# Optimization experiments

Measured on AMD Instinct MI355X. Metric: run time of the kernel, lower is better.

Reference implementation:

```python
import jax, jax.numpy as jnp
import numpy as np

S, B, E, H, DFF = 1024, 8, 1024, 16, 4096
D = E // H
EPS = 1e-5


def _layernorm(x, g, b):
    m = jnp.mean(x, axis=-1, keepdims=True)
    v = jnp.mean(jnp.square(x - m), axis=-1, keepdims=True)
    return (x - m) * jax.lax.rsqrt(v + EPS) * g + b


def setup_inputs() -> dict:
    key = jax.random.key(0)
    ks = jax.random.split(key, 6)
    return {
        "src": jax.random.normal(ks[0], (S, B, E), jnp.float32),
        "in_proj_w": jax.random.normal(ks[1], (3 * E, E), jnp.float32) * (E ** -0.5),
        "in_proj_b": jnp.zeros((3 * E,), jnp.float32),
        "out_w": jax.random.normal(ks[2], (E, E), jnp.float32) * (E ** -0.5),
        "out_b": jnp.zeros((E,), jnp.float32),
        "ln1_g": jnp.ones((E,), jnp.float32),
        "ln1_b": jnp.zeros((E,), jnp.float32),
        "ln2_g": jnp.ones((E,), jnp.float32),
        "ln2_b": jnp.zeros((E,), jnp.float32),
        "w1": jax.random.normal(ks[3], (DFF, E), jnp.float32) * (E ** -0.5),
        "b1": jnp.zeros((DFF,), jnp.float32),
        "w2": jax.random.normal(ks[4], (E, DFF), jnp.float32) * (DFF ** -0.5),
        "b2": jnp.zeros((E,), jnp.float32),
    }


def reference(src, in_proj_w, in_proj_b, out_w, out_b, ln1_g, ln1_b, ln2_g, ln2_b, w1, b1, w2, b2):
    # src: (S, B, E). Packed in-projection: qkv = src @ W^T + b, split into q,k,v.
    qkv = src @ in_proj_w.T + in_proj_b          # (S, B, 3E)
    q, k, v = jnp.split(qkv, 3, axis=-1)
    q = q.reshape(S, B, H, D)
    k = k.reshape(S, B, H, D)
    v = v.reshape(S, B, H, D)
    # Torch scales q by 1/sqrt(head_dim) before the bmm.
    scores = jnp.einsum("sbhd,tbhd->bhst", q * (D ** -0.5), k)   # (B, H, S, S)
    attn = jax.nn.softmax(scores, axis=-1)
    ctx = jnp.einsum("bhst,tbhd->sbhd", attn, v).reshape(S, B, E)
    attn_out = ctx @ out_w.T + out_b
    # Post-norm encoder layer (norm_first=False), dropout=0.
    x = _layernorm(src + attn_out, ln1_g, ln1_b)
    ff = jax.nn.relu(x @ w1.T + b1) @ w2.T + b2
    return _layernorm(x + ff, ln2_g, ln2_b)
```

## Files before the change

### kernel.cpp

```cpp
#include <hip/hip_runtime.h>

#define S_LEN 1024
#define BATCH 8
#define EMB   1024
#define NH    16
#define HD    64
#define FFD   4096
#define ROWS  (S_LEN*BATCH)

typedef __attribute__((ext_vector_type(8))) short  short8;
typedef __attribute__((ext_vector_type(4))) float  float4v;
typedef __attribute__((ext_vector_type(4))) unsigned int uint4v;

struct alignas(8) us4 { unsigned short x, y, z, w; };

__device__ __forceinline__ unsigned short f2bf(float f) {
    unsigned int u = __float_as_uint(f);
    u += 0x7fffu + ((u >> 16) & 1u);
    return (unsigned short)(u >> 16);
}
__device__ __forceinline__ float bf2f(unsigned short b) {
    return __uint_as_float((unsigned int)b << 16);
}
__device__ __forceinline__ unsigned int cvtpk_bf16(float lo, float hi) {
    unsigned int r;
    asm("v_cvt_pk_bf16_f32 %0, %1, %2" : "=v"(r) : "v"(lo), "v"(hi));
    return r;
}
__device__ __forceinline__ float exp2v(float x) {
    float r;
    asm("v_exp_f32 %0, %1" : "=v"(r) : "v"(x));
    return r;
}

__device__ __forceinline__ void gload_lds16(const void* g, void* l) {
    __builtin_amdgcn_global_load_lds(
        (const __attribute__((address_space(1))) unsigned int*)g,
        (__attribute__((address_space(3))) unsigned int*)l, 16, 0, 0);
}

__device__ __forceinline__ int swz(int row, int chunk) {
    return (row << 7) + ((chunk ^ (row & 7)) << 4);
}

__device__ __forceinline__ void xcd_decode(int id, int& lx, int& ly) {
    int k = id & 7, j = id >> 3;
    ly = k * 4 + (j & 3);
    lx = j >> 2;
}

__global__ __launch_bounds__(256) void cast_all(const float* __restrict__ s0, unsigned short* __restrict__ d0, int n0,
                                                const float* __restrict__ s1, unsigned short* __restrict__ d1, int n1,
                                                const float* __restrict__ s2, unsigned short* __restrict__ d2, int n2,
                                                const float* __restrict__ s3, unsigned short* __restrict__ d3, int n3,
                                                const float* __restrict__ s4, unsigned short* __restrict__ d4, int n4) {
    int i = blockIdx.x * 256 + threadIdx.x;
    const float* s; unsigned short* d;
    if (i < n0)                { s = s0; d = d0; }
    else if ((i -= n0) < n1)   { s = s1; d = d1; }
    else if ((i -= n1) < n2)   { s = s2; d = d2; }
    else if ((i -= n2) < n3)   { s = s3; d = d3; }
    else if ((i -= n3) < n4)   { s = s4; d = d4; }
    else return;
    float4 v = ((const float4*)s)[i];
    us4 o = { f2bf(v.x), f2bf(v.y), f2bf(v.z), f2bf(v.w) };
    ((us4*)d)[i] = o;
}

#define QSCALE 0.18033688011112042f
template <int MODE>
__global__ __launch_bounds__(512, 2) void gemm256(const unsigned short* __restrict__ A,
                                                  const unsigned short* __restrict__ Bw,
                                                  const float* __restrict__ bias,
                                                  unsigned short* __restrict__ outb,
                                                  int M, int N, int K) {
    __shared__ char lds[131072];
    const int tid = threadIdx.x, lane = tid & 63, w = tid >> 6;
    const int wr = w >> 2, wc = w & 3;
    int lx, ly;
    xcd_decode(blockIdx.x, lx, ly);
    const int m0 = ly * 256, n0 = lx * 256;
    const int nt = K >> 6;

    size_t baseA[2], baseB[2];
    int ldsOff[2];
#pragma unroll
    for (int q = 0; q < 2; ++q) {
        int ci = q * 512 + tid;
        int row = ci >> 3;
        int c = (ci & 7) ^ (row & 7);
        baseA[q] = (size_t)(m0 + row) * K + c * 8;
        baseB[q] = (size_t)(n0 + row) * K + c * 8;
        ldsOff[q] = ci * 16;
    }

    auto stage = [&](int kt, int which) {
        int ktc = kt < nt ? kt : 0;
        int slot = kt & 1;
        if (which < 2) {
#pragma unroll
            for (int q = 0; q < 2; ++q)
                gload_lds16(A + baseA[q] + (size_t)which * 128 * K + (size_t)ktc * 64,
                            lds + slot * 32768 + which * 16384 + ldsOff[q]);
        } else {
            int h = which - 2;
#pragma unroll
            for (int q = 0; q < 2; ++q)
                gload_lds16(Bw + baseB[q] + (size_t)h * 128 * K + (size_t)ktc * 64,
                            lds + 65536 + slot * 32768 + h * 16384 + ldsOff[q]);
        }
    };

    auto rdA = [&](int slot, int mh, int i, int mk) -> short8 {
        int arow = wr * 128 + mh * 64 + i * 16 + (lane & 15);
        return *(const short8*)(lds + slot * 32768 + swz(arow, mk * 4 + (lane >> 4)));
    };
    auto rdB = [&](int slot, int nh, int j, int mk) -> short8 {
        int brow = wc * 64 + nh * 32 + j * 16 + (lane & 15);
        return *(const short8*)(lds + 65536 + slot * 32768 + swz(brow, mk * 4 + (lane >> 4)));
    };

    float4v acc[8][4];
#pragma unroll
    for (int i = 0; i < 8; ++i)
#pragma unroll
        for (int j = 0; j < 4; ++j) acc[i][j] = (float4v){0.f, 0.f, 0.f, 0.f};

    short8 a[4][2], b[2][2][2];

    stage(0, 0); stage(0, 1); stage(0, 2); stage(0, 3);
    stage(1, 0);
    asm volatile("s_waitcnt vmcnt(2)" ::: "memory");
    __builtin_amdgcn_s_barrier();

#define MFMA16(MH, NH)                                                          \
    __builtin_amdgcn_s_setprio(1);                                              \
    _Pragma("unroll")                                                           \
    for (int i = 0; i < 4; ++i)                                                 \
        _Pragma("unroll")                                                       \
        for (int j = 0; j < 2; ++j) {                                           \
            acc[(MH)*4+i][(NH)*2+j] = __builtin_amdgcn_mfma_f32_16x16x32_bf16(  \
                a[i][0], b[NH][j][0], acc[(MH)*4+i][(NH)*2+j], 0, 0, 0);        \
            acc[(MH)*4+i][(NH)*2+j] = __builtin_amdgcn_mfma_f32_16x16x32_bf16(  \
                a[i][1], b[NH][j][1], acc[(MH)*4+i][(NH)*2+j], 0, 0, 0);        \
        }                                                                       \
    __builtin_amdgcn_s_setprio(0);

    for (int t = 0; t < nt; ++t) {
        const int slot = t & 1;
#pragma unroll
        for (int i = 0; i < 4; ++i) {
            a[i][0] = rdA(slot, 0, i, 0);
            a[i][1] = rdA(slot, 0, i, 1);
        }
#pragma unroll
        for (int j = 0; j < 2; ++j) {
            b[0][j][0] = rdB(slot, 0, j, 0);
            b[0][j][1] = rdB(slot, 0, j, 1);
        }
        stage(t + 1, 1);
        __builtin_amdgcn_s_barrier();
        asm volatile("s_waitcnt lgkmcnt(0)" ::: "memory");
        __builtin_amdgcn_sched_barrier(0);
        MFMA16(0, 0)
        __builtin_amdgcn_s_barrier();
#pragma unroll
        for (int j = 0; j < 2; ++j) {
            b[1][j][0] = rdB(slot, 1, j, 0);
            b[1][j][1] = rdB(slot, 1, j, 1);
        }
        stage(t + 1, 2);
        __builtin_amdgcn_s_barrier();
        asm volatile("s_waitcnt lgkmcnt(0)" ::: "memory");
        __builtin_amdgcn_sched_barrier(0);
        MFMA16(0, 1)
        __builtin_amdgcn_s_barrier();
#pragma unroll
        for (int i = 0; i < 4; ++i) {
            a[i][0] = rdA(slot, 1, i, 0);
            a[i][1] = rdA(slot, 1, i, 1);
        }
        stage(t + 1, 3);
        __builtin_amdgcn_s_barrier();
        asm volatile("s_waitcnt lgkmcnt(0)" ::: "memory");
        __builtin_amdgcn_sched_barrier(0);
        MFMA16(1, 1)
        __builtin_amdgcn_s_barrier();
        stage(t + 2, 0);
        MFMA16(1, 0)
        asm volatile("s_waitcnt vmcnt(2)" ::: "memory");
        __builtin_amdgcn_s_barrier();
    }
#undef MFMA16
    asm volatile("s_waitcnt vmcnt(0)" ::: "memory");

#pragma unroll
    for (int mi = 0; mi < 8; ++mi) {
#pragma unroll
        for (int nj = 0; nj < 4; ++nj) {
            int col = n0 + wc * 64 + nj * 16 + (lane & 15);
            float bv = bias[col];
#pragma unroll
            for (int r = 0; r < 4; ++r) {
                int row = m0 + wr * 128 + mi * 16 + (lane >> 4) * 4 + r;
                size_t idx = (size_t)row * N + col;
                float v = acc[mi][nj][r] + bv;
                if (MODE == 0) {
                    if (col < EMB) v *= QSCALE;
                    outb[idx] = f2bf(v);
                } else {
                    outb[idx] = f2bf(fmaxf(v, 0.f));
                }
            }
        }
    }
}

template <int MODE>
__global__ __launch_bounds__(512, 2) void gemm256n(const unsigned short* __restrict__ A,
                                                   const unsigned short* __restrict__ Bw,
                                                   const float* __restrict__ bias,
                                                   const float* __restrict__ res,
                                                   const unsigned short* __restrict__ resb,
                                                   float* __restrict__ outf,
                                                   int M, int N, int K) {
    __shared__ char lds[147456];
    const int tid = threadIdx.x, lane = tid & 63, w = tid >> 6;
    const int wr = w >> 1, wc = w & 1;
    int lx, ly;
    xcd_decode(blockIdx.x, lx, ly);
    const int m0 = ly * 256, n0 = lx * 128;
    const int nt = K >> 6;
    const int g = lane >> 4, qs = lane & 15;

    size_t baseA[4], baseB[2];
    int ldsOffA[4], ldsOffB[2];
#pragma unroll
    for (int q = 0; q < 4; ++q) {
        int ci = q * 512 + tid;
        int row = ci >> 3;
        int c = (ci & 7) ^ (row & 7);
        baseA[q] = (size_t)(m0 + row) * K + c * 8;
        ldsOffA[q] = ci * 16;
    }
#pragma unroll
    for (int q = 0; q < 2; ++q) {
        int ci = q * 512 + tid;
        int row = ci >> 3;
        int c = (ci & 7) ^ (row & 7);
        baseB[q] = (size_t)(n0 + row) * K + c * 8;
        ldsOffB[q] = ci * 16;
    }

    auto stage = [&](int kt) {
        int ktc = kt < nt ? kt : 0;
        int slot = kt % 3;
#pragma unroll
        for (int q = 0; q < 4; ++q)
            gload_lds16(A + baseA[q] + (size_t)ktc * 64,
                        lds + slot * 32768 + ldsOffA[q]);
#pragma unroll
        for (int q = 0; q < 2; ++q)
            gload_lds16(Bw + baseB[q] + (size_t)ktc * 64,
                        lds + 98304 + slot * 16384 + ldsOffB[q]);
    };

    auto rdA = [&](int slot, int i, int mk) -> short8 {
        int arow = wr * 64 + i * 16 + qs;
        return *(const short8*)(lds + slot * 32768 + swz(arow, mk * 4 + g));
    };
    auto rdB = [&](int slot, int j, int mk) -> short8 {
        int brow = wc * 64 + j * 16 + qs;
        return *(const short8*)(lds + 98304 + slot * 16384 + swz(brow, mk * 4 + g));
    };

    float4v acc[4][4];
#pragma unroll
    for (int i = 0; i < 4; ++i)
#pragma unroll
        for (int j = 0; j < 4; ++j) acc[i][j] = (float4v){0.f, 0.f, 0.f, 0.f};

    short8 a[4][2], b[4][2];

    stage(0); stage(1);
    asm volatile("s_waitcnt vmcnt(6)" ::: "memory");
    __builtin_amdgcn_s_barrier();

    for (int t = 0; t < nt; ++t) {
        const int slot = t % 3;
#pragma unroll
        for (int i = 0; i < 4; ++i) {
            a[i][0] = rdA(slot, i, 0);
            a[i][1] = rdA(slot, i, 1);
        }
#pragma unroll
        for (int j = 0; j < 4; ++j) {
            b[j][0] = rdB(slot, j, 0);
            b[j][1] = rdB(slot, j, 1);
        }
        stage(t + 2);
        asm volatile("s_waitcnt lgkmcnt(0)" ::: "memory");
        __builtin_amdgcn_sched_barrier(0);
        __builtin_amdgcn_s_setprio(1);
#pragma unroll
        for (int i = 0; i < 4; ++i)
#pragma unroll
            for (int j = 0; j < 4; ++j) {
                acc[i][j] = __builtin_amdgcn_mfma_f32_16x16x32_bf16(
                    a[i][0], b[j][0], acc[i][j], 0, 0, 0);
                acc[i][j] = __builtin_amdgcn_mfma_f32_16x16x32_bf16(
                    a[i][1], b[j][1], acc[i][j], 0, 0, 0);
            }
        __builtin_amdgcn_s_setprio(0);
        asm volatile("s_waitcnt vmcnt(6)" ::: "memory");
        __builtin_amdgcn_s_barrier();
    }
    asm volatile("s_waitcnt vmcnt(0)" ::: "memory");

#pragma unroll
    for (int mi = 0; mi < 4; ++mi) {
#pragma unroll
        for (int j = 0; j < 4; ++j) {
            int col = n0 + wc * 64 + j * 16 + qs;
            float bv = bias[col];
#pragma unroll
            for (int r = 0; r < 4; ++r) {
                int row = m0 + wr * 64 + mi * 16 + g * 4 + r;
                size_t idx = (size_t)row * N + col;
                float v = acc[mi][j][r] + bv;
                if (MODE == 1) outf[idx] = v + res[idx];
                else           outf[idx] = v + bf2f(resb[idx]);
            }
        }
    }
}

__global__ __launch_bounds__(256) void vtrans(const unsigned short* __restrict__ qkv,
                                              unsigned short* __restrict__ vt) {
    const int bh = blockIdx.y, b = bh >> 4, h = bh & 15;
    const int t0 = blockIdx.x * 64;
    const int tid = threadIdx.x;
    __shared__ unsigned short lds[64][72];
#pragma unroll
    for (int rep = 0; rep < 2; ++rep) {
        int slot = rep * 256 + tid;
        int row = slot >> 3, cc = slot & 7;
        const unsigned short* g =
            qkv + ((size_t)(t0 + row) * BATCH + b) * 3072 + 2 * EMB + h * 64 + cc * 8;
        *(uint4v*)&lds[row][cc * 8] = *(const uint4v*)g;
    }
    __syncthreads();
#pragma unroll
    for (int rep = 0; rep < 2; ++rep) {
        int slot = rep * 256 + tid;
        int d = slot >> 3, tc = slot & 7;
        unsigned short tmp[8] __attribute__((aligned(16)));
#pragma unroll
        for (int j = 0; j < 8; ++j) tmp[j] = lds[tc * 8 + j][d];
        unsigned short* g = vt + ((size_t)bh * 64 + d) * S_LEN + t0 + tc * 8;
        *(uint4v*)g = *(const uint4v*)tmp;
    }
}

__global__ __launch_bounds__(256, 6) void attn(const unsigned short* __restrict__ qkv,
                                               const unsigned short* __restrict__ vt,
                                               unsigned short* __restrict__ ctx) {
    __shared__ char Ks[64 * 128];
    __shared__ char Vs[64 * 128];
    __shared__ char QP[64 * 128];
    const int tid = threadIdx.x, lane = tid & 63, w = tid >> 6;
    const int bh = blockIdx.x & 127, b = bh >> 4, h = bh & 15;
    const int s0 = (blockIdx.x >> 7) * 64;
    const int g = lane >> 4, qs = lane & 15;

#pragma unroll
    for (int p = 0; p < 2; ++p) {
        int ci = p * 256 + tid;
        int row = ci >> 3, c = (ci & 7) ^ (row & 7);
        gload_lds16(qkv + ((size_t)(s0 + row) * BATCH + b) * 3072 + h * 64 + c * 8,
                    QP + (p * 256 + w * 64) * 16);
    }
    __syncthreads();

    short8 qa0 = *(const short8*)(QP + swz(w * 16 + qs, 0 * 4 + g));
    short8 qa1 = *(const short8*)(QP + swz(w * 16 + qs, 1 * 4 + g));
    asm volatile("s_waitcnt lgkmcnt(0)" ::: "memory");
    __builtin_amdgcn_sched_barrier(0);
    char* Ps = QP + w * 2048;

    float4v O[4];
#pragma unroll
    for (int df = 0; df < 4; ++df) O[df] = (float4v){0.f, 0.f, 0.f, 0.f};
    float m_s = -1e30f;
    float l_s = 0.f;

    for (int t0 = 0; t0 < S_LEN; t0 += 64) {
        __syncthreads();
#pragma unroll
        for (int p = 0; p < 2; ++p) {
            int ci = p * 256 + tid;
            int row = ci >> 3, c = (ci & 7) ^ (row & 7);
            gload_lds16(qkv + ((size_t)(t0 + row) * BATCH + b) * 3072 + EMB + h * 64 + c * 8,
                        Ks + (p * 256 + w * 64) * 16);
            gload_lds16(vt + ((size_t)bh * 64 + row) * S_LEN + t0 + c * 8,
                        Vs + (p * 256 + w * 64) * 16);
        }
        __syncthreads();

        float4v Sf[4];
#pragma unroll
        for (int tf = 0; tf < 4; ++tf) Sf[tf] = (float4v){0.f, 0.f, 0.f, 0.f};
#pragma unroll
        for (int tf = 0; tf < 4; ++tf) {
            int kr = tf * 16 + qs;
            short8 kb0 = *(const short8*)(Ks + swz(kr, 0 * 4 + g));
            short8 kb1 = *(const short8*)(Ks + swz(kr, 1 * 4 + g));
            Sf[tf] = __builtin_amdgcn_mfma_f32_16x16x32_bf16(kb0, qa0, Sf[tf], 0, 0, 0);
            Sf[tf] = __builtin_amdgcn_mfma_f32_16x16x32_bf16(kb1, qa1, Sf[tf], 0, 0, 0);
        }

        float mx = fmaxf(fmaxf(Sf[0][0], Sf[0][1]), fmaxf(Sf[0][2], Sf[0][3]));
#pragma unroll
        for (int tf = 1; tf < 4; ++tf)
            mx = fmaxf(mx, fmaxf(fmaxf(Sf[tf][0], Sf[tf][1]),
                                 fmaxf(Sf[tf][2], Sf[tf][3])));
        mx = fmaxf(mx, __shfl_xor(mx, 16));
        mx = fmaxf(mx, __shfl_xor(mx, 32));

        if (!__all(mx - m_s <= 8.0f)) {
            float mnew = fmaxf(m_s, mx);
            float alpha = exp2v(m_s - mnew);
            m_s = mnew;
            l_s *= alpha;
#pragma unroll
            for (int r = 0; r < 4; ++r) {
                float ar = __shfl(alpha, 4 * g + r);
#pragma unroll
                for (int df = 0; df < 4; ++df) O[df][r] *= ar;
            }
        }

        float rs = 0.f;
#pragma unroll
        for (int tf = 0; tf < 4; ++tf) {
            float p0 = exp2v(Sf[tf][0] - m_s);
            float p1 = exp2v(Sf[tf][1] - m_s);
            float p2 = exp2v(Sf[tf][2] - m_s);
            float p3 = exp2v(Sf[tf][3] - m_s);
            rs += (p0 + p1) + (p2 + p3);
            uint2 pk = make_uint2(cvtpk_bf16(p0, p1), cvtpk_bf16(p2, p3));
            *(uint2*)(Ps + (qs << 7) +
                      (((2 * tf + (g >> 1)) ^ (qs & 7)) << 4) + ((g & 1) << 3)) = pk;
        }
        rs += __shfl_xor(rs, 16);
        rs += __shfl_xor(rs, 32);
        l_s += rs;

        asm volatile("s_waitcnt lgkmcnt(0)" ::: "memory");
        __builtin_amdgcn_sched_barrier(0);

#pragma unroll
        for (int mk = 0; mk < 2; ++mk) {
            short8 pa = *(const short8*)(Ps + swz(qs, mk * 4 + g));
#pragma unroll
            for (int df = 0; df < 4; ++df) {
                int vr = df * 16 + qs;
                short8 vb = *(const short8*)(Vs + swz(vr, mk * 4 + g));
                O[df] = __builtin_amdgcn_mfma_f32_16x16x32_bf16(pa, vb, O[df], 0, 0, 0);
            }
        }
    }

    float inv = __builtin_amdgcn_rcpf(l_s);
#pragma unroll
    for (int r = 0; r < 4; ++r) {
        float ir = __shfl(inv, 4 * g + r);
#pragma unroll
        for (int df = 0; df < 4; ++df) {
            int srow = s0 + w * 16 + g * 4 + r;
            int d    = df * 16 + qs;
            ctx[((size_t)srow * BATCH + b) * EMB + h * 64 + d] = f2bf(O[df][r] * ir);
        }
    }
}

__global__ __launch_bounds__(256) void ln_ker(const float* __restrict__ y,
                                              const float* __restrict__ g,
                                              const float* __restrict__ bta,
                                              float* __restrict__ xo,
                                              unsigned short* __restrict__ xb) {
    const int row = blockIdx.x, tid = threadIdx.x, lane = tid & 63, w = tid >> 6;
    float4 v = ((const float4*)(y + (size_t)row * EMB))[tid];
    float s = v.x + v.y + v.z + v.w;
    float q = v.x * v.x + v.y * v.y + v.z * v.z + v.w * v.w;
#pragma unroll
    for (int m = 1; m < 64; m <<= 1) {
        s += __shfl_xor(s, m);
        q += __shfl_xor(q, m);
    }
    __shared__ float ps[4], pq[4];
    if (lane == 0) { ps[w] = s; pq[w] = q; }
    __syncthreads();
    s = ps[0] + ps[1] + ps[2] + ps[3];
    q = pq[0] + pq[1] + pq[2] + pq[3];
    float mean = s * (1.f / EMB);
    float var  = q * (1.f / EMB) - mean * mean;
    float rstd = rsqrtf(var + 1e-5f);
    float4 gv = ((const float4*)g)[tid];
    float4 bv = ((const float4*)bta)[tid];
    float4 o;
    o.x = (v.x - mean) * rstd * gv.x + bv.x;
    o.y = (v.y - mean) * rstd * gv.y + bv.y;
    o.z = (v.z - mean) * rstd * gv.z + bv.z;
    o.w = (v.w - mean) * rstd * gv.w + bv.w;
    if (xo) ((float4*)(xo + (size_t)row * EMB))[tid] = o;
    if (xb) {
        us4 ob = { f2bf(o.x), f2bf(o.y), f2bf(o.z), f2bf(o.w) };
        ((us4*)(xb + (size_t)row * EMB))[tid] = ob;
    }
}

extern "C" void kernel_launch(void* const* d_in, const int* in_sizes, int n_in,
                              void* d_out, int out_size, void* d_ws, size_t ws_size,
                              hipStream_t stream) {
    (void)in_sizes; (void)n_in; (void)out_size;
    const float* src       = (const float*)d_in[0];
    const float* in_proj_w = (const float*)d_in[1];
    const float* in_proj_b = (const float*)d_in[2];
    const float* out_w     = (const float*)d_in[3];
    const float* out_b     = (const float*)d_in[4];
    const float* ln1_g     = (const float*)d_in[5];
    const float* ln1_b     = (const float*)d_in[6];
    const float* ln2_g     = (const float*)d_in[7];
    const float* ln2_b     = (const float*)d_in[8];
    const float* w1        = (const float*)d_in[9];
    const float* b1        = (const float*)d_in[10];
    const float* w2        = (const float*)d_in[11];
    const float* b2        = (const float*)d_in[12];

    const size_t MB = 1u << 20;
    if (ws_size < 104 * MB) return;

    char* ws = (char*)d_ws;
    unsigned short* wqkvb = (unsigned short*)(ws);
    unsigned short* wob   = (unsigned short*)(ws + 6 * MB);
    unsigned short* w1b   = (unsigned short*)(ws + 8 * MB);
    unsigned short* w2b   = (unsigned short*)(ws + 16 * MB);
    unsigned short* qkvb  = (unsigned short*)(ws + 24 * MB);
    unsigned short* srcbf = (unsigned short*)(ws + 72 * MB);
    unsigned short* vtb   = (unsigned short*)(ws + 88 * MB);
    unsigned short* ctxb  = (unsigned short*)(ws + 72 * MB);
    unsigned short* xbf   = (unsigned short*)(ws + 24 * MB);
    unsigned short* hb    = (unsigned short*)(ws + 40 * MB);
    float*          yout  = (float*)d_out;

    const int c0 = ROWS * EMB / 4;
    const int c1 = 3 * EMB * EMB / 4;
    const int c2 = EMB * EMB / 4;
    const int c3 = FFD * EMB / 4;
    const int c4 = EMB * FFD / 4;
    const int ctot = c0 + c1 + c2 + c3 + c4;
    cast_all<<<ctot / 256, 256, 0, stream>>>(
        src, srcbf, c0, in_proj_w, wqkvb, c1, out_w, wob, c2,
        w1, w1b, c3, w2, w2b, c4);

    gemm256<0><<<(3 * EMB / 256) * 32, 512, 0, stream>>>(
        srcbf, wqkvb, in_proj_b, qkvb, ROWS, 3 * EMB, EMB);

    vtrans<<<dim3(S_LEN / 64, BATCH * NH), 256, 0, stream>>>(qkvb, vtb);

    attn<<<(S_LEN / 64) * BATCH * NH, 256, 0, stream>>>(qkvb, vtb, ctxb);

    gemm256n<1><<<(EMB / 128) * 32, 512, 0, stream>>>(
        ctxb, wob, out_b, src, nullptr, yout, ROWS, EMB, EMB);

    ln_ker<<<ROWS, 256, 0, stream>>>(yout, ln1_g, ln1_b, nullptr, xbf);

    gemm256<2><<<(FFD / 256) * 32, 512, 0, stream>>>(
        xbf, w1b, b1, hb, ROWS, FFD, EMB);

    gemm256n<3><<<(EMB / 128) * 32, 512, 0, stream>>>(
        hb, w2b, b2, nullptr, xbf, yout, ROWS, EMB, FFD);

    ln_ker<<<ROWS, 256, 0, stream>>>(yout, ln2_g, ln2_b, (float*)d_out, nullptr);
}
```

Measured before the change: 325.7 us.

## Triple-buffer A tile and cut barriers in 256x256 GEMM main loop

Replaces the 256x256 bf16 GEMM's four-phase loop, which had several barriers per k-step, with a loop that has one barrier per k-step. The A tile is triple-buffered and B double-buffered, using 160 KB of LDS, so loads run two steps ahead for A. Each wave now loads all four B fragments at once and runs two 32-MFMA bursts, reloading only the A fragments between them. This trades more LDS (160 KB) and more live registers for fewer synchronisations and deeper prefetch, and assumes the LDS allocation still fits on the device.

```diff
diff --git a/kernel.cpp b/kernel.cpp
--- a/kernel.cpp
+++ b/kernel.cpp
@@ -69,23 +69,24 @@
 
 #define QSCALE 0.18033688011112042f
 template <int MODE>
-__global__ __launch_bounds__(512, 2) void gemm256(const unsigned short* __restrict__ A,
-                                                  const unsigned short* __restrict__ Bw,
-                                                  const float* __restrict__ bias,
-                                                  unsigned short* __restrict__ outb,
-                                                  int M, int N, int K) {
-    __shared__ char lds[131072];
+__global__ __launch_bounds__(512, 2) void gemm256d(const unsigned short* __restrict__ A,
+                                                   const unsigned short* __restrict__ Bw,
+                                                   const float* __restrict__ bias,
+                                                   unsigned short* __restrict__ outb,
+                                                   int M, int N, int K) {
+    __shared__ char lds[163840];
     const int tid = threadIdx.x, lane = tid & 63, w = tid >> 6;
     const int wr = w >> 2, wc = w & 3;
+    const int g = lane >> 4, qs = lane & 15;
     int lx, ly;
     xcd_decode(blockIdx.x, lx, ly);
     const int m0 = ly * 256, n0 = lx * 256;
     const int nt = K >> 6;
 
-    size_t baseA[2], baseB[2];
-    int ldsOff[2];
-#pragma unroll
-    for (int q = 0; q < 2; ++q) {
+    size_t baseA[4], baseB[4];
+    int ldsOff[4];
+#pragma unroll
+    for (int q = 0; q < 4; ++q) {
         int ci = q * 512 + tid;
         int row = ci >> 3;
         int c = (ci & 7) ^ (row & 7);
@@ -94,30 +95,30 @@
         ldsOff[q] = ci * 16;
     }
 
-    auto stage = [&](int kt, int which) {
+    auto stageA = [&](int kt) {
+        int ktc = kt < nt ? kt : 0;
+        int slot = kt % 3;
+#pragma unroll
+        for (int q = 0; q < 4; ++q)
+            gload_lds16(A + baseA[q] + (size_t)ktc * 64,
+                        lds + slot * 32768 + ldsOff[q]);
+    };
+    auto stageB = [&](int kt) {
         int ktc = kt < nt ? kt : 0;
         int slot = kt & 1;
-        if (which < 2) {
-#pragma unroll
-            for (int q = 0; q < 2; ++q)
-                gload_lds16(A + baseA[q] + (size_t)which * 128 * K + (size_t)ktc * 64,
-                            lds + slot * 32768 + which * 16384 + ldsOff[q]);
-        } else {
-            int h = which - 2;
-#pragma unroll
-            for (int q = 0; q < 2; ++q)
-                gload_lds16(Bw + baseB[q] + (size_t)h * 128 * K + (size_t)ktc * 64,
-                            lds + 65536 + slot * 32768 + h * 16384 + ldsOff[q]);
-        }
-    };
-
-    auto rdA = [&](int slot, int mh, int i, int mk) -> short8 {
-        int arow = wr * 128 + mh * 64 + i * 16 + (lane & 15);
-        return *(const short8*)(lds + slot * 32768 + swz(arow, mk * 4 + (lane >> 4)));
-    };
-    auto rdB = [&](int slot, int nh, int j, int mk) -> short8 {
-        int brow = wc * 64 + nh * 32 + j * 16 + (lane & 15);
-        return *(const short8*)(lds + 65536 + slot * 32768 + swz(brow, mk * 4 + (lane >> 4)));
+#pragma unroll
+        for (int q = 0; q < 4; ++q)
+            gload_lds16(Bw + baseB[q] + (size_t)ktc * 64,
+                        lds + 98304 + slot * 32768 + ldsOff[q]);
+    };
+
+    auto rdA = [&](int slot, int ig, int mk) -> short8 {
+        int arow = wr * 128 + ig * 16 + qs;
+        return *(const short8*)(lds + slot * 32768 + swz(arow, mk * 4 + g));
+    };
+    auto rdB = [&](int slot, int j, int mk) -> short8 {
+        int brow = wc * 64 + j * 16 + qs;
+        return *(const short8*)(lds + 98304 + slot * 32768 + swz(brow, mk * 4 + g));
     };
 
     float4v acc[8][4];
@@ -126,83 +127,71 @@
 #pragma unroll
         for (int j = 0; j < 4; ++j) acc[i][j] = (float4v){0.f, 0.f, 0.f, 0.f};
 
-    short8 a[4][2], b[2][2][2];
-
-    stage(0, 0); stage(0, 1); stage(0, 2); stage(0, 3);
-    stage(1, 0);
-    asm volatile("s_waitcnt vmcnt(2)" ::: "memory");
+    short8 a[4][2], b[4][2];
+
+    stageA(0); stageB(0); stageA(1);
+    asm volatile("s_waitcnt vmcnt(4)" ::: "memory");
     __builtin_amdgcn_s_barrier();
 
-#define MFMA16(MH, NH)                                                          \
-    __builtin_amdgcn_s_setprio(1);                                              \
-    _Pragma("unroll")                                                           \
-    for (int i = 0; i < 4; ++i)                                                 \
-        _Pragma("unroll")                                                       \
-        for (int j = 0; j < 2; ++j) {                                           \
-            acc[(MH)*4+i][(NH)*2+j] = __builtin_amdgcn_mfma_f32_16x16x32_bf16(  \
-                a[i][0], b[NH][j][0], acc[(MH)*4+i][(NH)*2+j], 0, 0, 0);        \
-            acc[(MH)*4+i][(NH)*2+j] = __builtin_amdgcn_mfma_f32_16x16x32_bf16(  \
-                a[i][1], b[NH][j][1], acc[(MH)*4+i][(NH)*2+j], 0, 0, 0);        \
-        }                                                                       \
-    __builtin_amdgcn_s_setprio(0);
-
     for (int t = 0; t < nt; ++t) {
-        const int slot = t & 1;
+        const int sa = t % 3, sb = t & 1;
 #pragma unroll
         for (int i = 0; i < 4; ++i) {
-            a[i][0] = rdA(slot, 0, i, 0);
-            a[i][1] = rdA(slot, 0, i, 1);
-        }
-#pragma unroll
-        for (int j = 0; j < 2; ++j) {
-            b[0][j][0] = rdB(slot, 0, j, 0);
-            b[0][j][1] = rdB(slot, 0, j, 1);
-        }
-        stage(t + 1, 1);
-        __builtin_amdgcn_s_barrier();
+            a[i][0] = rdA(sa, i, 0);
+            a[i][1] = rdA(sa, i, 1);
+        }
+#pragma unroll
+        for (int j = 0; j < 4; ++j) {
+            b[j][0] = rdB(sb, j, 0);
+            b[j][1] = rdB(sb, j, 1);
+        }
+        stageB(t + 1);
+        stageA(t + 2);
         asm volatile("s_waitcnt lgkmcnt(0)" ::: "memory");
         __builtin_amdgcn_sched_barrier(0);
-        MFMA16(0, 0)
-        __builtin_amdgcn_s_barrier();
-#pragma unroll
-        for (int j = 0; j < 2; ++j) {
-            b[1][j][0] = rdB(slot, 1, j, 0);
-            b[1][j][1] = rdB(slot, 1, j, 1);
-        }
-        stage(t + 1, 2);
-        __builtin_amdgcn_s_barrier();
+        __builtin_amdgcn_s_setprio(1);
+#pragma unroll
+        for (int i = 0; i < 4; ++i)
+#pragma unroll
+            for (int j = 0; j < 4; ++j) {
+                acc[i][j] = __builtin_amdgcn_mfma_f32_16x16x32_bf16(
+                    a[i][0], b[j][0], acc[i][j], 0, 0, 0);
+                acc[i][j] = __builtin_amdgcn_mfma_f32_16x16x32_bf16(
+                    a[i][1], b[j][1], acc[i][j], 0, 0, 0);
+            }
+        __builtin_amdgcn_s_setprio(0);
+#pragma unroll
+        for (int i = 0; i < 4; ++i) {
+            a[i][0] = rdA(sa, 4 + i, 0);
+            a[i][1] = rdA(sa, 4 + i, 1);
+        }
         asm volatile("s_waitcnt lgkmcnt(0)" ::: "memory");
         __builtin_amdgcn_sched_barrier(0);
-        MFMA16(0, 1)
+        __builtin_amdgcn_s_setprio(1);
+#pragma unroll
+        for (int i = 0; i < 4; ++i)
+#pragma unroll
+            for (int j = 0; j < 4; ++j) {
+                acc[4 + i][j] = __builtin_amdgcn_mfma_f32_16x16x32_bf16(
+                    a[i][0], b[j][0], acc[4 + i][j], 0, 0, 0);
+                acc[4 + i][j] = __builtin_amdgcn_mfma_f32_16x16x32_bf16(
+                    a[i][1], b[j][1], acc[4 + i][j], 0, 0, 0);
+            }
+        __builtin_amdgcn_s_setprio(0);
+        asm volatile("s_waitcnt vmcnt(4)" ::: "memory");
         __builtin_amdgcn_s_barrier();
-#pragma unroll
-        for (int i = 0; i < 4; ++i) {
-            a[i][0] = rdA(slot, 1, i, 0);
-            a[i][1] = rdA(slot, 1, i, 1);
-        }
-        stage(t + 1, 3);
-        __builtin_amdgcn_s_barrier();
-        asm volatile("s_waitcnt lgkmcnt(0)" ::: "memory");
-        __builtin_amdgcn_sched_barrier(0);
-        MFMA16(1, 1)
-        __builtin_amdgcn_s_barrier();
-        stage(t + 2, 0);
-        MFMA16(1, 0)
-        asm volatile("s_waitcnt vmcnt(2)" ::: "memory");
-        __builtin_amdgcn_s_barrier();
-    }
-#undef MFMA16
+    }
     asm volatile("s_waitcnt vmcnt(0)" ::: "memory");
 
 #pragma unroll
     for (int mi = 0; mi < 8; ++mi) {
 #pragma unroll
         for (int nj = 0; nj < 4; ++nj) {
-            int col = n0 + wc * 64 + nj * 16 + (lane & 15);
+            int col = n0 + wc * 64 + nj * 16 + qs;
             float bv = bias[col];
 #pragma unroll
             for (int r = 0; r < 4; ++r) {
-                int row = m0 + wr * 128 + mi * 16 + (lane >> 4) * 4 + r;
+                int row = m0 + wr * 128 + mi * 16 + g * 4 + r;
                 size_t idx = (size_t)row * N + col;
                 float v = acc[mi][nj][r] + bv;
                 if (MODE == 0) {
@@ -564,7 +553,7 @@
         src, srcbf, c0, in_proj_w, wqkvb, c1, out_w, wob, c2,
         w1, w1b, c3, w2, w2b, c4);
 
-    gemm256<0><<<(3 * EMB / 256) * 32, 512, 0, stream>>>(
+    gemm256d<0><<<(3 * EMB / 256) * 32, 512, 0, stream>>>(
         srcbf, wqkvb, in_proj_b, qkvb, ROWS, 3 * EMB, EMB);
 
     vtrans<<<dim3(S_LEN / 64, BATCH * NH), 256, 0, stream>>>(qkvb, vtb);
@@ -576,7 +565,7 @@
 
     ln_ker<<<ROWS, 256, 0, stream>>>(yout, ln1_g, ln1_b, nullptr, xbf);
 
-    gemm256<2><<<(FFD / 256) * 32, 512, 0, stream>>>(
+    gemm256d<2><<<(FFD / 256) * 32, 512, 0, stream>>>(
         xbf, w1b, b1, hb, ROWS, FFD, EMB);
 
     gemm256n<3><<<(EMB / 128) * 32, 512, 0, stream>>>(
```

Measured after the change: 325.8 us. About the same (+0.0%).
